# Performance work log

Hardware: AMD Instinct MI355X
Metric: run time of the kernel (lower is better)

## Reference

```python
import jax, jax.numpy as jnp
import numpy as np

B, S, D, H = 2, 2048, 2048, 16
HD = D // H  # 128


def setup_inputs() -> dict:
    key = jax.random.key(0)
    ks = jax.random.split(key, 5)
    x = jax.random.normal(ks[0], (B, S, D), dtype=jnp.float32)
    scale = 1.0 / np.sqrt(D)
    wq = jax.random.normal(ks[1], (D, D), dtype=jnp.float32) * scale
    wk = jax.random.normal(ks[2], (D, D), dtype=jnp.float32) * scale
    wv = jax.random.normal(ks[3], (D, D), dtype=jnp.float32) * scale
    wo = jax.random.normal(ks[4], (D, D), dtype=jnp.float32) * scale
    # RoPE frequencies: theta = 10000, freqs_cis[t, j] = exp(i * t / theta^(2j/HD))
    inv_freq = 1.0 / (10000.0 ** (jnp.arange(0, HD, 2, dtype=jnp.float32) / HD))  # [HD/2]
    t = jnp.arange(S, dtype=jnp.float32)
    ang = jnp.outer(t, inv_freq)  # [S, HD/2]
    freqs_cos = jnp.cos(ang)
    freqs_sin = jnp.sin(ang)
    # Additive causal mask [S, S]
    neg = jnp.float32(-1e9)
    mask = jnp.triu(jnp.full((S, S), neg, dtype=jnp.float32), k=1)
    return {"x": x, "wq": wq, "wk": wk, "wv": wv, "wo": wo,
            "freqs_cos": freqs_cos, "freqs_sin": freqs_sin,
            "mask": mask, "start_pos": 0}


def _rope(t, cos, sin):
    # t: [B, S, H, HD]; cos/sin: [S, HD/2] broadcast as [1, S, 1, HD/2]
    tr = t.reshape(t.shape[:-1] + (HD // 2, 2))
    xr, xi = tr[..., 0], tr[..., 1]
    c = cos[None, :, None, :]
    s = sin[None, :, None, :]
    out_r = xr * c - xi * s
    out_i = xr * s + xi * c
    return jnp.stack([out_r, out_i], axis=-1).reshape(t.shape)


def reference(x, wq, wk, wv, wo, freqs_cos, freqs_sin, mask, start_pos):
    bsz, seqlen, _ = x.shape
    # nn.Linear: y = x @ W.T
    xq = jnp.einsum('bsd,ed->bse', x, wq).reshape(bsz, seqlen, H, HD)
    xk = jnp.einsum('bsd,ed->bse', x, wk).reshape(bsz, seqlen, H, HD)
    xv = jnp.einsum('bsd,ed->bse', x, wv).reshape(bsz, seqlen, H, HD)
    xq = _rope(xq, freqs_cos, freqs_sin)
    xk = _rope(xk, freqs_cos, freqs_sin)
    # [B, H, S, HD]
    xq = xq.transpose(0, 2, 1, 3)
    xk = xk.transpose(0, 2, 1, 3)
    xv = xv.transpose(0, 2, 1, 3)
    scores = jnp.einsum('bhqd,bhkd->bhqk', xq, xk) / jnp.sqrt(jnp.float32(HD))
    scores = scores + mask[None, None, :, :]
    probs = jax.nn.softmax(scores.astype(jnp.float32), axis=-1).astype(xq.dtype)
    out = jnp.einsum('bhqk,bhkd->bhqd', probs, xv)
    out = out.transpose(0, 2, 1, 3).reshape(bsz, seqlen, H * HD)
    return jnp.einsum('bse,de->bsd', out, wo)
```

## Files before the change

kernel.cpp:

```cpp
#include <hip/hip_runtime.h>


#define SQ 2048
#define DQ 2048
#define HQ 16
#define HDQ 128

typedef short bf16x8 __attribute__((ext_vector_type(8)));
typedef float f32x4 __attribute__((ext_vector_type(4)));

#define WAITVM8 asm volatile("s_waitcnt vmcnt(8)" ::: "memory")
#define WAITVM0 asm volatile("s_waitcnt vmcnt(0)" ::: "memory")

__device__ __forceinline__ short f2bf(float f) {
  union { float f; unsigned u; } v; v.f = f;
  unsigned r = (v.u + 0x7FFFu + ((v.u >> 16) & 1u)) >> 16;
  return (short)r;
}
__device__ __forceinline__ float bf2f(short b) {
  union { unsigned u; float f; } v; v.u = ((unsigned)(unsigned short)b) << 16;
  return v.f;
}
__device__ __forceinline__ void gload_lds16(const void* g, void* l) {
  __builtin_amdgcn_global_load_lds(
      (const __attribute__((address_space(1))) void*)g,
      (__attribute__((address_space(3))) void*)l, 16, 0, 0);
}

__global__ void cvt_kernel(const float* __restrict__ in, short* __restrict__ out, int nvec) {
  int i = blockIdx.x * blockDim.x + threadIdx.x;
  if (i >= nvec) return;
  const f32x4* p = (const f32x4*)in + (size_t)i * 2;
  f32x4 a = p[0], b = p[1];
  bf16x8 o;
  o[0] = f2bf(a[0]); o[1] = f2bf(a[1]); o[2] = f2bf(a[2]); o[3] = f2bf(a[3]);
  o[4] = f2bf(b[0]); o[5] = f2bf(b[1]); o[6] = f2bf(b[2]); o[7] = f2bf(b[3]);
  *((bf16x8*)out + i) = o;
}

__global__ void rope_kernel(short* __restrict__ t, const float* __restrict__ cosT,
                            const float* __restrict__ sinT, float scale, int nvec) {
  int i = blockIdx.x * blockDim.x + threadIdx.x;
  if (i >= nvec) return;
  size_t off = (size_t)i * 8;
  int hd0 = (int)(off & 127);
  int s = (int)((off >> 7) & 2047);
  bf16x8 v = *((const bf16x8*)(t + off));
  f32x4 c  = *(const f32x4*)(cosT + (size_t)s * 64 + (hd0 >> 1));
  f32x4 sn = *(const f32x4*)(sinT + (size_t)s * 64 + (hd0 >> 1));
  bf16x8 o;
#pragma unroll
  for (int p = 0; p < 4; ++p) {
    float xr = bf2f(v[2 * p]), xi = bf2f(v[2 * p + 1]);
    o[2 * p]     = f2bf((xr * c[p] - xi * sn[p]) * scale);
    o[2 * p + 1] = f2bf((xr * sn[p] + xi * c[p]) * scale);
  }
  *((bf16x8*)(t + off)) = o;
}

__global__ void vtrans_kernel(const short* __restrict__ vb, short* __restrict__ vtb) {
  __shared__ __align__(16) short tile[64][72];
  int bh = blockIdx.z, s0 = blockIdx.y * 64, d0 = blockIdx.x * 64;
  int tid = threadIdx.x;
#pragma unroll
  for (int it = 0; it < 2; ++it) {
    int vi = it * 256 + tid;
    int r = vi >> 3, c8 = (vi & 7) * 8;
    bf16x8 v = *(const bf16x8*)&vb[((size_t)bh * SQ + s0 + r) * HDQ + d0 + c8];
    *(bf16x8*)&tile[r][c8] = v;
  }
  __syncthreads();
#pragma unroll
  for (int it = 0; it < 2; ++it) {
    int vi = it * 256 + tid;
    int d = vi >> 3, s8 = (vi & 7) * 8;
    bf16x8 o;
#pragma unroll
    for (int j = 0; j < 8; ++j) o[j] = tile[s8 + j][d];
    *(bf16x8*)&vtb[((size_t)bh * HDQ + d0 + d) * SQ + s0 + s8] = o;
  }
}

template <int MODE>
__global__ __launch_bounds__(256, 2) void gemm_bt(const short* __restrict__ A,
                                                  const short* __restrict__ W,
                                                  short* __restrict__ oQ, short* __restrict__ oK,
                                                  short* __restrict__ oV, float* __restrict__ oF) {
  const int K = DQ;
  __shared__ __align__(16) short As[128 * 32];
  __shared__ __align__(16) short Bs[128 * 32];
  int n0 = blockIdx.x * 128, m0 = blockIdx.y * 128;
  const short* Bw = (MODE == 0) ? (W + (size_t)blockIdx.z * DQ * DQ) : W;
  int tid = threadIdx.x, w = tid >> 6, lane = tid & 63;
  int wr = w >> 1, wc = w & 1;
  int ar = lane >> 2, acol = (lane & 3) * 8;
  f32x4 acc[4][4] = {};
  int lra = wr * 64 + (lane & 15), lrb = wc * 64 + (lane & 15), kc = (lane >> 4) * 8;
  for (int k0 = 0; k0 < K; k0 += 32) {
    __syncthreads();
#pragma unroll
    for (int i = 0; i < 2; ++i) {
      int c = w * 2 + i;
      int r = c * 16 + ar;
      gload_lds16(A + (size_t)(m0 + r) * K + k0 + acol, &As[c * 512]);
      gload_lds16(Bw + (size_t)(n0 + r) * K + k0 + acol, &Bs[c * 512]);
    }
    __syncthreads();
    bf16x8 af[4], bfr[4];
#pragma unroll
    for (int f = 0; f < 4; ++f) {
      af[f] = *(const bf16x8*)&As[(lra + f * 16) * 32 + kc];
      bfr[f] = *(const bf16x8*)&Bs[(lrb + f * 16) * 32 + kc];
    }
#pragma unroll
    for (int mf = 0; mf < 4; ++mf)
#pragma unroll
      for (int nf = 0; nf < 4; ++nf)
        acc[mf][nf] = __builtin_amdgcn_mfma_f32_16x16x32_bf16(af[mf], bfr[nf], acc[mf][nf], 0, 0, 0);
  }
  short* oT = nullptr;
  if (MODE == 0) oT = (blockIdx.z == 0) ? oQ : (blockIdx.z == 1) ? oK : oV;
#pragma unroll
  for (int mf = 0; mf < 4; ++mf) {
    int mb = m0 + wr * 64 + mf * 16 + (lane >> 4) * 4;
#pragma unroll
    for (int nf = 0; nf < 4; ++nf) {
      int n = n0 + wc * 64 + nf * 16 + (lane & 15);
#pragma unroll
      for (int j = 0; j < 4; ++j) {
        int m = mb + j;
        float v = acc[mf][nf][j];
        if (MODE == 0) {
          int b = m >> 11, s = m & 2047, h = n >> 7, hd = n & 127;
          oT[(((size_t)(b * HQ + h)) * SQ + s) * HDQ + hd] = f2bf(v);
        } else {
          oF[(size_t)m * DQ + n] = v;
        }
      }
    }
  }
}

__device__ __forceinline__ void stage_kv(const short* kbase, const short* vbase, int k0,
                                         short* KsB, short* VtB, int w, int lane) {
#pragma unroll
  for (int i = 0; i < 4; ++i) {
    int c = w * 4 + i;
    int r = c * 4 + (lane >> 4);
    int col = (lane & 15) * 8;
    gload_lds16(kbase + (size_t)(k0 + r) * HDQ + (col ^ ((r & 7) << 3)), KsB + c * 512);
    int d = c * 8 + (lane >> 3);
    int jj = (lane & 7) * 8;
    gload_lds16(vbase + (size_t)d * SQ + k0 + (jj ^ ((d & 7) << 3)), VtB + c * 512);
  }
}

__global__ __launch_bounds__(256, 2) void flash_kernel(const short* __restrict__ qb,
                                                       const short* __restrict__ kb,
                                                       const short* __restrict__ vtb,
                                                       short* __restrict__ ab) {
  __shared__ __align__(16) short Ks[2][64 * 128];
  __shared__ __align__(16) short Vt[2][128 * 64];
  __shared__ __align__(16) short Pl[4][16 * 68];
  int x = blockIdx.x, bh = blockIdx.y;
  int qt = (bh & 8) ? (31 - x) : x;
  int q0 = qt * 64;
  int tid = threadIdx.x, w = tid >> 6, lane = tid & 63;
  const short* qbase = qb + (size_t)bh * SQ * HDQ;
  const short* kbase = kb + (size_t)bh * SQ * HDQ;
  const short* vbase = vtb + (size_t)bh * HDQ * SQ;
  int b = bh >> 4, h = bh & 15;

  bf16x8 qf[4];
  {
    int qr = q0 + w * 16 + (lane & 15);
    int kq = (lane >> 4) * 8;
#pragma unroll
    for (int c = 0; c < 4; ++c)
      qf[c] = *(const bf16x8*)&qbase[(size_t)qr * HDQ + c * 32 + kq];
  }
  f32x4 oacc[8] = {};
  f32x4 m_st = f32x4{-1e30f, -1e30f, -1e30f, -1e30f};
  f32x4 l_st = f32x4{0.f, 0.f, 0.f, 0.f};
  int nt = qt + 1;
  stage_kv(kbase, vbase, 0, Ks[0], Vt[0], w, lane);
#pragma unroll 1
  for (int t = 0; t < nt; ++t) {
    int cur = t & 1;
    int k0 = t * 64;
    __builtin_amdgcn_s_barrier();
    if (t + 1 < nt) {
      stage_kv(kbase, vbase, (t + 1) * 64, Ks[cur ^ 1], Vt[cur ^ 1], w, lane);
      WAITVM8;
    } else {
      WAITVM0;
    }
    __builtin_amdgcn_s_barrier();
    f32x4 sacc[4] = {};
    __builtin_amdgcn_s_setprio(1);
#pragma unroll
    for (int nf = 0; nf < 4; ++nf) {
      int rk = nf * 16 + (lane & 15);
#pragma unroll
      for (int cc = 0; cc < 4; ++cc) {
        int ck = cc * 32 + (lane >> 4) * 8;
        bf16x8 kf = *(const bf16x8*)&Ks[cur][rk * 128 + (ck ^ ((rk & 7) << 3))];
        sacc[nf] = __builtin_amdgcn_mfma_f32_16x16x32_bf16(qf[cc], kf, sacc[nf], 0, 0, 0);
      }
    }
    __builtin_amdgcn_s_setprio(0);
    if (t == nt - 1) {
#pragma unroll
      for (int nf = 0; nf < 4; ++nf)
#pragma unroll
        for (int j = 0; j < 4; ++j) {
          int q = q0 + w * 16 + (lane >> 4) * 4 + j;
          int k = k0 + nf * 16 + (lane & 15);
          if (k > q) sacc[nf][j] -= 1e9f;
        }
    }
    f32x4 mt = sacc[0];
#pragma unroll
    for (int nf = 1; nf < 4; ++nf)
#pragma unroll
      for (int j = 0; j < 4; ++j) mt[j] = fmaxf(mt[j], sacc[nf][j]);
#pragma unroll
    for (int d = 1; d < 16; d <<= 1)
#pragma unroll
      for (int j = 0; j < 4; ++j) mt[j] = fmaxf(mt[j], __shfl_xor(mt[j], d));
    f32x4 mn, al;
#pragma unroll
    for (int j = 0; j < 4; ++j) {
      mn[j] = fmaxf(m_st[j], mt[j]);
      al[j] = exp2f(m_st[j] - mn[j]);
    }
#pragma unroll
    for (int df = 0; df < 8; ++df) oacc[df] *= al;
#pragma unroll
    for (int nf = 0; nf < 4; ++nf)
#pragma unroll
      for (int j = 0; j < 4; ++j) {
        float p = exp2f(sacc[nf][j] - mn[j]);
        l_st[j] = l_st[j] * ((nf == 0) ? al[j] : 1.0f) + p;
        Pl[w][((lane >> 4) * 4 + j) * 68 + nf * 16 + (lane & 15)] = f2bf(p);
      }
    m_st = mn;
    __builtin_amdgcn_s_setprio(1);
#pragma unroll
    for (int cc = 0; cc < 2; ++cc) {
      bf16x8 pf = *(const bf16x8*)&Pl[w][(lane & 15) * 68 + cc * 32 + (lane >> 4) * 8];
#pragma unroll
      for (int df = 0; df < 8; ++df) {
        int rd = df * 16 + (lane & 15);
        int cv = cc * 32 + (lane >> 4) * 8;
        bf16x8 vf = *(const bf16x8*)&Vt[cur][rd * 64 + (cv ^ ((rd & 7) << 3))];
        oacc[df] = __builtin_amdgcn_mfma_f32_16x16x32_bf16(pf, vf, oacc[df], 0, 0, 0);
      }
    }
    __builtin_amdgcn_s_setprio(0);
  }
#pragma unroll
  for (int d = 1; d < 16; d <<= 1)
#pragma unroll
    for (int j = 0; j < 4; ++j) l_st[j] += __shfl_xor(l_st[j], d);
  f32x4 inv;
#pragma unroll
  for (int j = 0; j < 4; ++j) inv[j] = 1.0f / l_st[j];
#pragma unroll
  for (int df = 0; df < 8; ++df)
#pragma unroll
    for (int j = 0; j < 4; ++j) {
      int q = q0 + w * 16 + (lane >> 4) * 4 + j;
      int dd = df * 16 + (lane & 15);
      ab[((size_t)b * SQ + q) * DQ + h * HDQ + dd] = f2bf(oacc[df][j] * inv[j]);
    }
}

extern "C" void kernel_launch(void* const* d_in, const int* in_sizes, int n_in,
                              void* d_out, int out_size, void* d_ws, size_t ws_size,
                              hipStream_t stream) {
  (void)in_sizes; (void)n_in; (void)out_size; (void)ws_size;
  const float* x  = (const float*)d_in[0];
  const float* wq = (const float*)d_in[1];
  const float* wk = (const float*)d_in[2];
  const float* wv = (const float*)d_in[3];
  const float* wo = (const float*)d_in[4];
  const float* fc = (const float*)d_in[5];
  const float* fs = (const float*)d_in[6];
  float* out = (float*)d_out;

  short* xb  = (short*)d_ws;
  short* wqb = xb + (size_t)8388608;
  short* wkb = wqb + (size_t)4194304;
  short* wvb = wkb + (size_t)4194304;
  short* wob = wvb + (size_t)4194304;
  short* qb  = wob + (size_t)4194304;
  short* kb  = qb + (size_t)8388608;
  short* ab  = kb + (size_t)8388608;
  short* vb  = (short*)d_out;
  short* vtb = vb + (size_t)8388608;

  cvt_kernel<<<4096, 256, 0, stream>>>(x, xb, 1048576);
  cvt_kernel<<<2048, 256, 0, stream>>>(wq, wqb, 524288);
  cvt_kernel<<<2048, 256, 0, stream>>>(wk, wkb, 524288);
  cvt_kernel<<<2048, 256, 0, stream>>>(wv, wvb, 524288);
  cvt_kernel<<<2048, 256, 0, stream>>>(wo, wob, 524288);

  gemm_bt<0><<<dim3(16, 32, 3), 256, 0, stream>>>(xb, wqb, qb, kb, vb, nullptr);

  rope_kernel<<<4096, 256, 0, stream>>>(qb, fc, fs, 0.12751744779976827f, 1048576);
  rope_kernel<<<4096, 256, 0, stream>>>(kb, fc, fs, 1.0f, 1048576);

  vtrans_kernel<<<dim3(2, 32, 32), 256, 0, stream>>>(vb, vtb);

  flash_kernel<<<dim3(32, 32), 256, 0, stream>>>(qb, kb, vtb, ab);

  gemm_bt<1><<<dim3(16, 32, 1), 256, 0, stream>>>(ab, wob, nullptr, nullptr, nullptr, out);
}
```

Measured before the change: 334.3 us.

## Shrink flash KV tile to 32, compute S transposed, skip masked tiles per wave

The flash attention kernel now stages 32-key tiles instead of 64, which halves LDS use and raises the occupancy hint from 2 to 4 blocks per CU. QK^T is computed with swapped MFMA operands so each lane owns one query row. That reduces the row max and sum reductions to two cross-lane shuffles, and P is written to LDS as packed bf16x4 with an XOR swizzle. Each wave skips key tiles that lie fully above its causal diagonal, so the causal skip is finer-grained. The cost is twice as many barrier-synchronised loop iterations and extra shuffles to broadcast the rescale factors.

```diff
diff --git a/kernel.cpp b/kernel.cpp
--- a/kernel.cpp
+++ b/kernel.cpp
@@ -7,9 +7,10 @@
 #define HDQ 128
 
 typedef short bf16x8 __attribute__((ext_vector_type(8)));
+typedef short bf16x4 __attribute__((ext_vector_type(4)));
 typedef float f32x4 __attribute__((ext_vector_type(4)));
 
-#define WAITVM8 asm volatile("s_waitcnt vmcnt(8)" ::: "memory")
+#define WAITVM4 asm volatile("s_waitcnt vmcnt(4)" ::: "memory")
 #define WAITVM0 asm volatile("s_waitcnt vmcnt(0)" ::: "memory")
 
 __device__ __forceinline__ short f2bf(float f) {
@@ -141,138 +142,136 @@
   }
 }
 
-__device__ __forceinline__ void stage_kv(const short* kbase, const short* vbase, int k0,
-                                         short* KsB, short* VtB, int w, int lane) {
-#pragma unroll
-  for (int i = 0; i < 4; ++i) {
-    int c = w * 4 + i;
-    int r = c * 4 + (lane >> 4);
-    int col = (lane & 15) * 8;
-    gload_lds16(kbase + (size_t)(k0 + r) * HDQ + (col ^ ((r & 7) << 3)), KsB + c * 512);
-    int d = c * 8 + (lane >> 3);
-    int jj = (lane & 7) * 8;
-    gload_lds16(vbase + (size_t)d * SQ + k0 + (jj ^ ((d & 7) << 3)), VtB + c * 512);
-  }
-}
-
-__global__ __launch_bounds__(256, 2) void flash_kernel(const short* __restrict__ qb,
+__device__ __forceinline__ void stage_kv32(const short* kbase, const short* vbase, int k0,
+                                           short* KsB, short* VtB, int w, int lane) {
+#pragma unroll
+  for (int i = 0; i < 2; ++i) {
+    int c = i * 4 + w;
+    int ch = c * 64 + lane;
+    int r = ch >> 4, c8 = (ch & 15) * 8;
+    gload_lds16(kbase + (size_t)(k0 + r) * HDQ + (c8 ^ ((r & 7) << 3)), KsB + c * 512);
+    int d = ch >> 2, k8 = (ch & 3) * 8;
+    gload_lds16(vbase + (size_t)d * SQ + k0 + (k8 ^ (((d >> 1) & 3) << 3)), VtB + c * 512);
+  }
+}
+
+__global__ __launch_bounds__(256, 4) void flash_kernel(const short* __restrict__ qb,
                                                        const short* __restrict__ kb,
                                                        const short* __restrict__ vtb,
                                                        short* __restrict__ ab) {
-  __shared__ __align__(16) short Ks[2][64 * 128];
-  __shared__ __align__(16) short Vt[2][128 * 64];
-  __shared__ __align__(16) short Pl[4][16 * 68];
+  __shared__ __align__(16) short Ks[2][32 * 128];
+  __shared__ __align__(16) short Vt[2][128 * 32];
+  __shared__ __align__(16) short Pl[4][16 * 32];
   int x = blockIdx.x, bh = blockIdx.y;
   int qt = (bh & 8) ? (31 - x) : x;
   int q0 = qt * 64;
   int tid = threadIdx.x, w = tid >> 6, lane = tid & 63;
+  int g = lane >> 4, qcol = lane & 15;
+  int qw0 = q0 + w * 16;
   const short* qbase = qb + (size_t)bh * SQ * HDQ;
   const short* kbase = kb + (size_t)bh * SQ * HDQ;
   const short* vbase = vtb + (size_t)bh * HDQ * SQ;
   int b = bh >> 4, h = bh & 15;
 
   bf16x8 qf[4];
-  {
-    int qr = q0 + w * 16 + (lane & 15);
-    int kq = (lane >> 4) * 8;
-#pragma unroll
-    for (int c = 0; c < 4; ++c)
-      qf[c] = *(const bf16x8*)&qbase[(size_t)qr * HDQ + c * 32 + kq];
-  }
+#pragma unroll
+  for (int cc = 0; cc < 4; ++cc)
+    qf[cc] = *(const bf16x8*)&qbase[(size_t)(qw0 + qcol) * HDQ + cc * 32 + g * 8];
+
   f32x4 oacc[8] = {};
-  f32x4 m_st = f32x4{-1e30f, -1e30f, -1e30f, -1e30f};
-  f32x4 l_st = f32x4{0.f, 0.f, 0.f, 0.f};
-  int nt = qt + 1;
-  stage_kv(kbase, vbase, 0, Ks[0], Vt[0], w, lane);
+  float m_st = -1e30f, l_st = 0.f;
+  int nt = 2 * qt + 2;
+  stage_kv32(kbase, vbase, 0, Ks[0], Vt[0], w, lane);
 #pragma unroll 1
   for (int t = 0; t < nt; ++t) {
     int cur = t & 1;
-    int k0 = t * 64;
+    int k0 = t * 32;
     __builtin_amdgcn_s_barrier();
     if (t + 1 < nt) {
-      stage_kv(kbase, vbase, (t + 1) * 64, Ks[cur ^ 1], Vt[cur ^ 1], w, lane);
-      WAITVM8;
+      stage_kv32(kbase, vbase, (t + 1) * 32, Ks[cur ^ 1], Vt[cur ^ 1], w, lane);
+      WAITVM4;
     } else {
       WAITVM0;
     }
     __builtin_amdgcn_s_barrier();
-    f32x4 sacc[4] = {};
+    if (k0 > qw0 + 15) continue;
+    f32x4 sacc[2] = {};
     __builtin_amdgcn_s_setprio(1);
 #pragma unroll
-    for (int nf = 0; nf < 4; ++nf) {
-      int rk = nf * 16 + (lane & 15);
+    for (int nf = 0; nf < 2; ++nf) {
+      int rk = nf * 16 + qcol;
 #pragma unroll
       for (int cc = 0; cc < 4; ++cc) {
-        int ck = cc * 32 + (lane >> 4) * 8;
+        int ck = cc * 32 + g * 8;
         bf16x8 kf = *(const bf16x8*)&Ks[cur][rk * 128 + (ck ^ ((rk & 7) << 3))];
-        sacc[nf] = __builtin_amdgcn_mfma_f32_16x16x32_bf16(qf[cc], kf, sacc[nf], 0, 0, 0);
+        sacc[nf] = __builtin_amdgcn_mfma_f32_16x16x32_bf16(kf, qf[cc], sacc[nf], 0, 0, 0);
       }
     }
     __builtin_amdgcn_s_setprio(0);
-    if (t == nt - 1) {
-#pragma unroll
-      for (int nf = 0; nf < 4; ++nf)
+    int q = qw0 + qcol;
+    if (k0 + 31 > qw0) {
+#pragma unroll
+      for (int nf = 0; nf < 2; ++nf)
 #pragma unroll
         for (int j = 0; j < 4; ++j) {
-          int q = q0 + w * 16 + (lane >> 4) * 4 + j;
-          int k = k0 + nf * 16 + (lane & 15);
-          if (k > q) sacc[nf][j] -= 1e9f;
+          int k = k0 + nf * 16 + g * 4 + j;
+          if (k > q) sacc[nf][j] = -1e9f;
         }
     }
-    f32x4 mt = sacc[0];
-#pragma unroll
-    for (int nf = 1; nf < 4; ++nf)
-#pragma unroll
-      for (int j = 0; j < 4; ++j) mt[j] = fmaxf(mt[j], sacc[nf][j]);
-#pragma unroll
-    for (int d = 1; d < 16; d <<= 1)
-#pragma unroll
-      for (int j = 0; j < 4; ++j) mt[j] = fmaxf(mt[j], __shfl_xor(mt[j], d));
-    f32x4 mn, al;
+    float mt = fmaxf(fmaxf(fmaxf(sacc[0][0], sacc[0][1]), fmaxf(sacc[0][2], sacc[0][3])),
+                     fmaxf(fmaxf(sacc[1][0], sacc[1][1]), fmaxf(sacc[1][2], sacc[1][3])));
+    mt = fmaxf(mt, __shfl_xor(mt, 16));
+    mt = fmaxf(mt, __shfl_xor(mt, 32));
+    float mn = fmaxf(m_st, mt);
+    float al = exp2f(m_st - mn);
+    float p0[4], p1[4];
+    float ls = 0.f;
+#pragma unroll
+    for (int j = 0; j < 4; ++j) { p0[j] = exp2f(sacc[0][j] - mn); ls += p0[j]; }
+#pragma unroll
+    for (int j = 0; j < 4; ++j) { p1[j] = exp2f(sacc[1][j] - mn); ls += p1[j]; }
+    l_st = l_st * al + ls;
+    m_st = mn;
+    int sw = (qcol & 3) * 8;
+    {
+      bf16x4 pk;
+      pk[0] = f2bf(p0[0]); pk[1] = f2bf(p0[1]); pk[2] = f2bf(p0[2]); pk[3] = f2bf(p0[3]);
+      *(bf16x4*)&Pl[w][qcol * 32 + ((g * 4) ^ sw)] = pk;
+      pk[0] = f2bf(p1[0]); pk[1] = f2bf(p1[1]); pk[2] = f2bf(p1[2]); pk[3] = f2bf(p1[3]);
+      *(bf16x4*)&Pl[w][qcol * 32 + ((16 + g * 4) ^ sw)] = pk;
+    }
+    f32x4 alv;
+    alv[0] = __shfl(al, g * 4 + 0);
+    alv[1] = __shfl(al, g * 4 + 1);
+    alv[2] = __shfl(al, g * 4 + 2);
+    alv[3] = __shfl(al, g * 4 + 3);
+#pragma unroll
+    for (int df = 0; df < 8; ++df) oacc[df] *= alv;
+    bf16x8 pf = *(const bf16x8*)&Pl[w][qcol * 32 + ((g * 8) ^ sw)];
+    __builtin_amdgcn_s_setprio(1);
+#pragma unroll
+    for (int df = 0; df < 8; ++df) {
+      int rd = df * 16 + qcol;
+      bf16x8 vf = *(const bf16x8*)&Vt[cur][rd * 32 + ((g * 8) ^ (((rd >> 1) & 3) << 3))];
+      oacc[df] = __builtin_amdgcn_mfma_f32_16x16x32_bf16(pf, vf, oacc[df], 0, 0, 0);
+    }
+    __builtin_amdgcn_s_setprio(0);
+  }
+  l_st += __shfl_xor(l_st, 16);
+  l_st += __shfl_xor(l_st, 32);
+  float inv = 1.0f / l_st;
+  f32x4 invv;
+  invv[0] = __shfl(inv, g * 4 + 0);
+  invv[1] = __shfl(inv, g * 4 + 1);
+  invv[2] = __shfl(inv, g * 4 + 2);
+  invv[3] = __shfl(inv, g * 4 + 3);
+#pragma unroll
+  for (int df = 0; df < 8; ++df)
 #pragma unroll
     for (int j = 0; j < 4; ++j) {
-      mn[j] = fmaxf(m_st[j], mt[j]);
-      al[j] = exp2f(m_st[j] - mn[j]);
-    }
-#pragma unroll
-    for (int df = 0; df < 8; ++df) oacc[df] *= al;
-#pragma unroll
-    for (int nf = 0; nf < 4; ++nf)
-#pragma unroll
-      for (int j = 0; j < 4; ++j) {
-        float p = exp2f(sacc[nf][j] - mn[j]);
-        l_st[j] = l_st[j] * ((nf == 0) ? al[j] : 1.0f) + p;
-        Pl[w][((lane >> 4) * 4 + j) * 68 + nf * 16 + (lane & 15)] = f2bf(p);
-      }
-    m_st = mn;
-    __builtin_amdgcn_s_setprio(1);
-#pragma unroll
-    for (int cc = 0; cc < 2; ++cc) {
-      bf16x8 pf = *(const bf16x8*)&Pl[w][(lane & 15) * 68 + cc * 32 + (lane >> 4) * 8];
-#pragma unroll
-      for (int df = 0; df < 8; ++df) {
-        int rd = df * 16 + (lane & 15);
-        int cv = cc * 32 + (lane >> 4) * 8;
-        bf16x8 vf = *(const bf16x8*)&Vt[cur][rd * 64 + (cv ^ ((rd & 7) << 3))];
-        oacc[df] = __builtin_amdgcn_mfma_f32_16x16x32_bf16(pf, vf, oacc[df], 0, 0, 0);
-      }
-    }
-    __builtin_amdgcn_s_setprio(0);
-  }
-#pragma unroll
-  for (int d = 1; d < 16; d <<= 1)
-#pragma unroll
-    for (int j = 0; j < 4; ++j) l_st[j] += __shfl_xor(l_st[j], d);
-  f32x4 inv;
-#pragma unroll
-  for (int j = 0; j < 4; ++j) inv[j] = 1.0f / l_st[j];
-#pragma unroll
-  for (int df = 0; df < 8; ++df)
-#pragma unroll
-    for (int j = 0; j < 4; ++j) {
-      int q = q0 + w * 16 + (lane >> 4) * 4 + j;
-      int dd = df * 16 + (lane & 15);
-      ab[((size_t)b * SQ + q) * DQ + h * HDQ + dd] = f2bf(oacc[df][j] * inv[j]);
+      int qq = qw0 + g * 4 + j;
+      int dd = df * 16 + qcol;
+      ab[((size_t)b * SQ + qq) * DQ + h * HDQ + dd] = f2bf(oacc[df][j] * invv[j]);
     }
 }
 
```

Measured after the change: 308.8 us. -7.6%, faster.
